# Optimization experiments

Measured on AMD Instinct MI355X. Metric: run time of the kernel, lower is better.

Reference implementation:

```python
import math
import jax, jax.numpy as jnp
import numpy as np

# ---- model dims ----
D = 4096          # hidden_size
N = 32            # num_attention_heads (== num_key_value_heads)
Q_LORA = 1536
KV_LORA = 512
QK_NOPE = 128
QK_ROPE = 64
QK_HEAD = QK_NOPE + QK_ROPE   # 192
V_HEAD = 128
EPS = 1e-6
T = 2048

# ---- yarn rope constants ----
ROPE_THETA = 10000.0
FACTOR = 40.0
ORIG_MAX = 4096
BETA_FAST = 32.0
BETA_SLOW = 1.0
MSCALE = 1.0
MSCALE_ALL_DIM = 1.0


def _yarn_get_mscale(scale, mscale):
    if scale <= 1.0:
        return 1.0
    return 0.1 * mscale * math.log(scale) + 1.0

# softmax scale: qk_head_dim^-0.5 * yarn_mscale^2 (rope_mscale_all_dim = 1.0)
YARN_MSCALE = _yarn_get_mscale(FACTOR, MSCALE_ALL_DIM)
SM_SCALE = QK_HEAD ** (-0.5) * YARN_MSCALE ** 2


def _yarn_cos_sin(positions):
    """DeepSeek yarn scaled rotary embeddings. positions: int [T]."""
    half = QK_ROPE // 2
    pow_ = np.arange(0, QK_ROPE, 2, dtype=np.float64) / QK_ROPE
    pos_freqs = ROPE_THETA ** pow_
    inv_extra = 1.0 / pos_freqs
    inv_inter = 1.0 / (FACTOR * pos_freqs)

    def corr_dim(n_rot):
        return (QK_ROPE * math.log(ORIG_MAX / (n_rot * 2 * math.pi))) / (2 * math.log(ROPE_THETA))

    low = max(math.floor(corr_dim(BETA_FAST)), 0)
    high = min(math.ceil(corr_dim(BETA_SLOW)), QK_ROPE - 1)
    ramp = np.clip((np.arange(half, dtype=np.float64) - low) / max(high - low, 1e-3), 0.0, 1.0)
    mask = 1.0 - ramp  # 1 where extrapolation
    inv_freq = inv_inter * (1.0 - mask) + inv_extra * mask
    inv_freq = jnp.asarray(inv_freq, jnp.float32)

    mscale_coef = _yarn_get_mscale(FACTOR, MSCALE) / _yarn_get_mscale(FACTOR, MSCALE_ALL_DIM)
    t = positions.astype(jnp.float32)
    freqs = t[:, None] * inv_freq[None, :]          # [T, half]
    return jnp.cos(freqs) * mscale_coef, jnp.sin(freqs) * mscale_coef


def _apply_rope(x_tnh, cos, sin):
    """Neox-style (split halves) rope. x: [T, N, QK_ROPE]; cos/sin: [T, half]."""
    half = QK_ROPE // 2
    x1, x2 = x_tnh[..., :half], x_tnh[..., half:]
    c, s = cos[:, None, :], sin[:, None, :]
    return jnp.concatenate([x1 * c - x2 * s, x1 * s + x2 * c], axis=-1)


def _rms_norm(x, scale, eps=EPS):
    var = jnp.mean(jnp.square(x), axis=-1, keepdims=True)
    return x * jax.lax.rsqrt(var + eps) * scale


def setup_inputs() -> dict:
    key = jax.random.key(0)
    ks = jax.random.split(key, 8)
    std = 0.02
    return {
        "x": jax.random.normal(ks[0], (T, D), jnp.float32),
        "positions": jnp.arange(T, dtype=jnp.int32),
        "w_q_down": jax.random.normal(ks[1], (D, Q_LORA), jnp.float32) * std,
        "q_norm_scale": jnp.ones((Q_LORA,), jnp.float32),
        "w_q_up": jax.random.normal(ks[2], (Q_LORA, N, QK_HEAD), jnp.float32) * std,
        "w_kv_down": jax.random.normal(ks[3], (D, KV_LORA + QK_ROPE), jnp.float32) * std,
        "kv_norm_scale": jnp.ones((KV_LORA,), jnp.float32),
        "w_kv_up": jax.random.normal(ks[4], (KV_LORA, N, QK_NOPE + V_HEAD), jnp.float32) * std,
        "w_o": jax.random.normal(ks[5], (N, V_HEAD, D), jnp.float32) * std,
    }


def reference(x, positions, w_q_down, q_norm_scale, w_q_up, w_kv_down,
              kv_norm_scale, w_kv_up, w_o):
    cos, sin = _yarn_cos_sin(positions)

    # ---- q projection (low rank) ----
    q_ta = _rms_norm(jnp.einsum('td,da->ta', x, w_q_down), q_norm_scale)
    q_tnh = jnp.einsum('ta,anh->tnh', q_ta, w_q_up)            # [T,N,192]
    q_rope = _apply_rope(q_tnh[..., QK_NOPE:], cos, sin)
    q_tnh = jnp.concatenate([q_tnh[..., :QK_NOPE], q_rope], axis=-1)

    # ---- kv projection (compressed latent) ----
    kv_sa = jnp.einsum('sd,da->sa', x, w_kv_down)              # [T, KV_LORA+64]
    k_rope = _apply_rope(kv_sa[:, None, KV_LORA:], cos, sin)   # [T,1,64]
    k_rope = jnp.broadcast_to(k_rope, (x.shape[0], N, QK_ROPE))
    kv_lat = _rms_norm(kv_sa[..., :KV_LORA], kv_norm_scale)
    kv_nope = jnp.einsum('sa,anh->snh', kv_lat, w_kv_up)       # [T,N,256]
    k_snh = jnp.concatenate([kv_nope[..., :QK_NOPE], k_rope], axis=-1)
    v_snh = kv_nope[..., QK_NOPE:]

    # ---- causal attention (prefill; padding to 128-multiple is a no-op) ----
    scores = jnp.einsum('tnh,snh->nts', q_tnh, k_snh) * SM_SCALE
    tpos = jnp.arange(x.shape[0])
    causal = tpos[:, None] >= tpos[None, :]
    scores = jnp.where(causal[None, :, :], scores, jnp.finfo(scores.dtype).min)
    probs = jax.nn.softmax(scores, axis=-1)
    out_tnh = jnp.einsum('nts,snh->tnh', probs, v_snh)

    # ---- output projection ----
    return jnp.einsum('tnh,nhd->td', out_tnh, w_o)
```

## Files before the change

kernel.cpp:

```cpp
#include <hip/hip_runtime.h>
#include <math.h>
#include <stdint.h>

#define T_    2048
#define D_    4096
#define NH_   32
#define QL_   1536
#define KVL_  512
#define ROPE_ 64
#define NOPE_ 128
#define HQK_  192
#define HV_   128
#define KVD_  576
#define NCAT_ 2112

typedef __bf16 bf16x8 __attribute__((ext_vector_type(8)));
typedef __bf16 bf16x4 __attribute__((ext_vector_type(4)));
typedef float f32x4 __attribute__((ext_vector_type(4)));

__device__ __forceinline__ void gload_lds16(const __bf16* g, __bf16* l) {
  __builtin_amdgcn_global_load_lds(
      (const __attribute__((address_space(1))) void*)g,
      (__attribute__((address_space(3))) void*)l, 16, 0, 0);
}

template <typename OutT>
__global__ __launch_bounds__(256, 3) void mfma_gemm_kernel(
    const __bf16* __restrict__ A, const __bf16* __restrict__ Bt,
    OutT* __restrict__ C, int M, int Ncols, int K) {
  __shared__ __bf16 As[128 * 64];
  __shared__ __bf16 Bs[128 * 64];
  const int tid = threadIdx.x;
  const int lane = tid & 63;
  const int w = tid >> 6;
  const int wm = w >> 1, wn = w & 1;
  const int lg = lane >> 4, lj = lane & 15;
  const int bm = blockIdx.y * 128;
  const int bn = blockIdx.x * 128;

  const __bf16* ga[4]; const __bf16* gb[4];
  int ldsoff[4];
  #pragma unroll
  for (int i = 0; i < 4; ++i) {
    int task = i * 256 + tid;
    int r = task >> 3, cl = task & 7;
    int cg = cl ^ (r & 7);
    ga[i] = A  + (size_t)(bm + r) * K + cg * 8;
    gb[i] = Bt + (size_t)(bn + r) * K + cg * 8;
    ldsoff[i] = (i * 256 + w * 64) * 8;
  }

  f32x4 acc[4][4];
  #pragma unroll
  for (int mi = 0; mi < 4; ++mi)
    #pragma unroll
    for (int ni = 0; ni < 4; ++ni) acc[mi][ni] = (f32x4){0.f, 0.f, 0.f, 0.f};

  for (int k0 = 0; k0 < K; k0 += 64) {
    __syncthreads();
    #pragma unroll
    for (int i = 0; i < 4; ++i) gload_lds16(ga[i] + k0, &As[ldsoff[i]]);
    #pragma unroll
    for (int i = 0; i < 4; ++i) gload_lds16(gb[i] + k0, &Bs[ldsoff[i]]);
    __syncthreads();
    #pragma unroll
    for (int kh = 0; kh < 2; ++kh) {
      bf16x8 af[4], bfr[4];
      #pragma unroll
      for (int i = 0; i < 4; ++i) {
        int ra = wm * 64 + i * 16 + lj;
        af[i] = *(const bf16x8*)&As[ra * 64 + ((((kh << 2) + lg) ^ (ra & 7)) << 3)];
      }
      #pragma unroll
      for (int i = 0; i < 4; ++i) {
        int rb = wn * 64 + i * 16 + lj;
        bfr[i] = *(const bf16x8*)&Bs[rb * 64 + ((((kh << 2) + lg) ^ (rb & 7)) << 3)];
      }
      #pragma unroll
      for (int mi = 0; mi < 4; ++mi)
        #pragma unroll
        for (int ni = 0; ni < 4; ++ni)
          acc[mi][ni] = __builtin_amdgcn_mfma_f32_16x16x32_bf16(af[mi], bfr[ni], acc[mi][ni], 0, 0, 0);
    }
  }

  #pragma unroll
  for (int mi = 0; mi < 4; ++mi) {
    #pragma unroll
    for (int r = 0; r < 4; ++r) {
      int row = bm + wm * 64 + mi * 16 + lg * 4 + r;
      #pragma unroll
      for (int ni = 0; ni < 4; ++ni) {
        int col = bn + wn * 64 + ni * 16 + lj;
        if (col < Ncols) C[(size_t)row * Ncols + col] = (OutT)acc[mi][ni][r];
      }
    }
  }
}

__global__ __launch_bounds__(256) void transpose_bf16_kernel(
    const float* __restrict__ B, __bf16* __restrict__ Bt, int K, int N) {
  __shared__ float tile[64][65];
  int n0 = blockIdx.x * 64, k0 = blockIdx.y * 64;
  int tid = threadIdx.x;
  int kr = tid >> 4, nc = (tid & 15) * 4;
  #pragma unroll
  for (int i = 0; i < 4; ++i) {
    int k = kr + i * 16;
    float4 v = make_float4(0.f, 0.f, 0.f, 0.f);
    if (n0 + nc < N) v = *(const float4*)(B + (size_t)(k0 + k) * N + n0 + nc);
    tile[k][nc + 0] = v.x; tile[k][nc + 1] = v.y;
    tile[k][nc + 2] = v.z; tile[k][nc + 3] = v.w;
  }
  __syncthreads();
  int nl = tid >> 4, k4 = (tid & 15) * 4;
  #pragma unroll
  for (int i = 0; i < 4; ++i) {
    int nn = nl + i * 16;
    bf16x4 o;
    o[0] = (__bf16)tile[k4 + 0][nn]; o[1] = (__bf16)tile[k4 + 1][nn];
    o[2] = (__bf16)tile[k4 + 2][nn]; o[3] = (__bf16)tile[k4 + 3][nn];
    *(bf16x4*)(Bt + (size_t)(n0 + nn) * K + k0 + k4) = o;
  }
}

__global__ __launch_bounds__(256) void conv_bf16_kernel(
    const float* __restrict__ in, __bf16* __restrict__ out, int n8) {
  int i = blockIdx.x * 256 + threadIdx.x;
  if (i >= n8) return;
  float4 a = *(const float4*)(in + (size_t)i * 8);
  float4 b = *(const float4*)(in + (size_t)i * 8 + 4);
  bf16x8 v;
  v[0] = (__bf16)a.x; v[1] = (__bf16)a.y; v[2] = (__bf16)a.z; v[3] = (__bf16)a.w;
  v[4] = (__bf16)b.x; v[5] = (__bf16)b.y; v[6] = (__bf16)b.z; v[7] = (__bf16)b.w;
  *(bf16x8*)(out + (size_t)i * 8) = v;
}

__global__ __launch_bounds__(256) void rmsnorm_bf16_kernel(
    const float* __restrict__ in, __bf16* __restrict__ out,
    const float* __restrict__ scale, int len, int in_stride) {
  int row = blockIdx.x;
  const float* x = in + (size_t)row * in_stride;
  __bf16* y = out + (size_t)row * len;
  float ss = 0.f;
  for (int i = threadIdx.x; i < len; i += 256) { float v = x[i]; ss += v * v; }
  __shared__ float red[4];
  #pragma unroll
  for (int o = 32; o > 0; o >>= 1) ss += __shfl_down(ss, o, 64);
  int wid = threadIdx.x >> 6, lane = threadIdx.x & 63;
  if (lane == 0) red[wid] = ss;
  __syncthreads();
  if (threadIdx.x == 0) {
    float t = red[0] + red[1] + red[2] + red[3];
    red[0] = 1.0f / sqrtf(t / (float)len + 1e-6f);
  }
  __syncthreads();
  float r = red[0];
  for (int i = threadIdx.x; i < len; i += 256) y[i] = (__bf16)(x[i] * r * scale[i]);
}

struct InvFreq { float f[32]; };
__global__ __launch_bounds__(256) void rope_table_kernel(
    const int* __restrict__ pos, float* __restrict__ cosT, float* __restrict__ sinT,
    InvFreq invf) {
  int idx = blockIdx.x * 256 + threadIdx.x;
  if (idx >= T_ * 32) return;
  int t = idx >> 5, i = idx & 31;
  float fr = (float)pos[t] * invf.f[i];
  cosT[idx] = cosf(fr);
  sinT[idx] = sinf(fr);
}

__global__ __launch_bounds__(256) void rope_q_kernel(
    __bf16* __restrict__ q, const float* __restrict__ cosT, const float* __restrict__ sinT) {
  int idx = blockIdx.x * 256 + threadIdx.x;
  if (idx >= T_ * NH_ * 32) return;
  int i = idx & 31;
  int tn = idx >> 5;
  int t = tn >> 5;
  __bf16* b = q + (size_t)tn * HQK_ + NOPE_;
  float x1 = (float)b[i], x2 = (float)b[i + 32];
  float c = cosT[t * 32 + i], s = sinT[t * 32 + i];
  b[i]      = (__bf16)(x1 * c - x2 * s);
  b[i + 32] = (__bf16)(x1 * s + x2 * c);
}

__global__ __launch_bounds__(256) void rope_k_kernel(
    const float* __restrict__ src, int stride, const float* __restrict__ cosT,
    const float* __restrict__ sinT, __bf16* __restrict__ k_rope) {
  int idx = blockIdx.x * 256 + threadIdx.x;
  if (idx >= T_ * 32) return;
  int t = idx >> 5, i = idx & 31;
  const float* b = src + (size_t)t * stride;
  float x1 = b[i], x2 = b[i + 32];
  float c = cosT[idx], s = sinT[idx];
  k_rope[t * 64 + i]      = (__bf16)(x1 * c - x2 * s);
  k_rope[t * 64 + i + 32] = (__bf16)(x1 * s + x2 * c);
}

__global__ __launch_bounds__(256) void prep_vt_kernel(
    const __bf16* __restrict__ kv_nopeb, __bf16* __restrict__ Vt) {
  __shared__ __bf16 tile[64][136];
  int s0 = blockIdx.x * 64;
  int n = blockIdx.y;
  int tid = threadIdx.x;
  #pragma unroll
  for (int i = 0; i < 4; ++i) {
    int idx = tid + i * 256;
    int s = idx >> 4, c = idx & 15;
    bf16x8 v = *(const bf16x8*)(kv_nopeb + ((size_t)(s0 + s) * NH_ + n) * 256 + NOPE_ + c * 8);
    *(bf16x8*)&tile[s][c * 8] = v;
  }
  __syncthreads();
  #pragma unroll
  for (int i = 0; i < 8; ++i) {
    int idx = tid + i * 256;
    int h = idx >> 4, s4 = (idx & 15) * 4;
    bf16x4 v;
    v[0] = tile[s4 + 0][h]; v[1] = tile[s4 + 1][h];
    v[2] = tile[s4 + 2][h]; v[3] = tile[s4 + 3][h];
    *(bf16x4*)(Vt + ((size_t)n * HV_ + h) * T_ + s0 + s4) = v;
  }
}

__global__ __launch_bounds__(256) void attn_mfma_kernel(
    const __bf16* __restrict__ q_tnh, const __bf16* __restrict__ kv_nopeb,
    const __bf16* __restrict__ k_rope, const __bf16* __restrict__ Vt,
    __bf16* __restrict__ attn_out, float sm_scale) {
  __shared__ __bf16 KsL[2][24 * 32 * 8];
  __shared__ __bf16 VsL[2][4 * 128 * 8];
  __shared__ __bf16 Ps[4][16 * 64];
  const int tid = threadIdx.x;
  const int lane = tid & 63;
  const int w = tid >> 6;
  const int id = blockIdx.x;
  const int j = id >> 3;
  const int qt = 31 - (j >> 2);
  const int n = (id & 7) * 4 + (j & 3);
  const int t0 = qt * 64;
  const int lg = lane >> 4;
  const int lj = lane & 15;
  const int rowbase = t0 + w * 16;

  const __bf16* kbase[3]; size_t kstep[3]; int klds[3];
  #pragma unroll
  for (int i = 0; i < 3; ++i) {
    int task = i * 256 + tid;
    int c = task >> 5, s = task & 31;
    if (c < 16) { kbase[i] = kv_nopeb + ((size_t)s * NH_ + n) * 256 + c * 8; kstep[i] = (size_t)32 * NH_ * 256; }
    else        { kbase[i] = k_rope + (size_t)s * ROPE_ + (c - 16) * 8;      kstep[i] = (size_t)32 * ROPE_; }
    klds[i] = (i * 256 + w * 64) * 8;
  }
  const __bf16* vbase[2]; int vlds[2];
  #pragma unroll
  for (int i = 0; i < 2; ++i) {
    int task = i * 256 + tid;
    int c = task >> 7, h = task & 127;
    vbase[i] = Vt + ((size_t)n * HV_ + h) * T_ + c * 8;
    vlds[i] = (i * 256 + w * 64) * 8;
  }

  #define STAGE(tileIdx, bufIdx)                                               \
    do {                                                                       \
      __bf16* kb_ = &KsL[bufIdx][0];                                           \
      __bf16* vb_ = &VsL[bufIdx][0];                                           \
      _Pragma("unroll")                                                        \
      for (int i_ = 0; i_ < 3; ++i_)                                           \
        gload_lds16(kbase[i_] + (size_t)(tileIdx) * kstep[i_], kb_ + klds[i_]);\
      _Pragma("unroll")                                                        \
      for (int i_ = 0; i_ < 2; ++i_)                                           \
        gload_lds16(vbase[i_] + (size_t)(tileIdx) * 32, vb_ + vlds[i_]);       \
    } while (0)

  STAGE(0, 0);

  bf16x8 qf[6];
  {
    int t = t0 + w * 16 + lj;
    const __bf16* qp = q_tnh + ((size_t)t * NH_ + n) * HQK_;
    #pragma unroll
    for (int kk = 0; kk < 6; ++kk) {
      bf16x8 raw = *(const bf16x8*)(qp + kk * 32 + lg * 8);
      bf16x8 v;
      #pragma unroll
      for (int i = 0; i < 8; ++i) v[i] = (__bf16)((float)raw[i] * sm_scale);
      qf[kk] = v;
    }
  }

  f32x4 O[8];
  #pragma unroll
  for (int nb = 0; nb < 8; ++nb) O[nb] = (f32x4){0.f, 0.f, 0.f, 0.f};
  float m_r[4], l_r[4];
  #pragma unroll
  for (int r = 0; r < 4; ++r) { m_r[r] = -1e30f; l_r[r] = 0.f; }

  __syncthreads();

  const int nst = 2 * (qt + 1);
  #pragma unroll 1
  for (int st = 0; st < nst; ++st) {
    const int s0 = st * 32;
    const int cur = st & 1;
    if (st + 1 < nst) STAGE(st + 1, cur ^ 1);
    const __bf16* kb = &KsL[cur][0];
    const __bf16* vb = &VsL[cur][0];

    if (s0 <= rowbase + 15) {
      f32x4 S[2];
      __builtin_amdgcn_s_setprio(1);
      #pragma unroll
      for (int sb = 0; sb < 2; ++sb) {
        f32x4 acc = (f32x4){0.f, 0.f, 0.f, 0.f};
        int srow = sb * 16 + lj;
        #pragma unroll
        for (int kk = 0; kk < 6; ++kk) {
          int c = kk * 4 + lg;
          bf16x8 b = *(const bf16x8*)&kb[(c * 32 + srow) * 8];
          acc = __builtin_amdgcn_mfma_f32_16x16x32_bf16(qf[kk], b, acc, 0, 0, 0);
        }
        S[sb] = acc;
      }
      __builtin_amdgcn_s_setprio(0);
      if (s0 + 31 > rowbase) {
        #pragma unroll
        for (int sb = 0; sb < 2; ++sb)
          #pragma unroll
          for (int r = 0; r < 4; ++r) {
            int row = rowbase + lg * 4 + r;
            int col = s0 + sb * 16 + lj;
            if (col > row) S[sb][r] = -1e30f;
          }
      }
      #pragma unroll
      for (int r = 0; r < 4; ++r) {
        float mx = fmaxf(S[0][r], S[1][r]);
        mx = fmaxf(mx, __shfl_xor(mx, 1));
        mx = fmaxf(mx, __shfl_xor(mx, 2));
        mx = fmaxf(mx, __shfl_xor(mx, 4));
        mx = fmaxf(mx, __shfl_xor(mx, 8));
        float mnew = fmaxf(m_r[r], mx);
        float corr = __expf(m_r[r] - mnew);
        m_r[r] = mnew;
        float psum = 0.f;
        #pragma unroll
        for (int sb = 0; sb < 2; ++sb) {
          float pp = __expf(S[sb][r] - mnew);
          S[sb][r] = pp;
          psum += pp;
        }
        l_r[r] = l_r[r] * corr + psum;
        #pragma unroll
        for (int nb = 0; nb < 8; ++nb) O[nb][r] = O[nb][r] * corr;
      }
      #pragma unroll
      for (int sb = 0; sb < 2; ++sb) {
        int sl = sb * 16 + lj;
        int c = sl >> 3;
        #pragma unroll
        for (int r = 0; r < 4; ++r) {
          int rw = lg * 4 + r;
          Ps[w][rw * 64 + ((c ^ (rw & 7)) << 3) + (sl & 7)] = (__bf16)S[sb][r];
        }
      }
      {
        bf16x8 pa = *(const bf16x8*)&Ps[w][lj * 64 + ((lg ^ (lj & 7)) << 3)];
        __builtin_amdgcn_s_setprio(1);
        #pragma unroll
        for (int nb = 0; nb < 8; ++nb) {
          int h = nb * 16 + lj;
          bf16x8 bv = *(const bf16x8*)&vb[(lg * 128 + h) * 8];
          O[nb] = __builtin_amdgcn_mfma_f32_16x16x32_bf16(pa, bv, O[nb], 0, 0, 0);
        }
        __builtin_amdgcn_s_setprio(0);
      }
    }
    __syncthreads();
  }

  #pragma unroll
  for (int r = 0; r < 4; ++r) {
    float lsum = l_r[r];
    lsum += __shfl_xor(lsum, 1);
    lsum += __shfl_xor(lsum, 2);
    lsum += __shfl_xor(lsum, 4);
    lsum += __shfl_xor(lsum, 8);
    float inv = 1.0f / lsum;
    int t = t0 + w * 16 + lg * 4 + r;
    __bf16* dst = attn_out + ((size_t)t * NH_ + n) * HV_;
    #pragma unroll
    for (int nb = 0; nb < 8; ++nb) dst[nb * 16 + lj] = (__bf16)(O[nb][r] * inv);
  }
  #undef STAGE
}

static void compute_inv_freq(float* out) {
  const double theta = 10000.0, factor = 40.0;
  const double PI = 3.14159265358979323846;
  const int rot = ROPE_;
  double low_d  = rot * log(4096.0 / (32.0 * 2.0 * PI)) / (2.0 * log(theta));
  double high_d = rot * log(4096.0 / ( 1.0 * 2.0 * PI)) / (2.0 * log(theta));
  double low = floor(low_d);  if (low < 0) low = 0;
  double high = ceil(high_d); if (high > rot - 1) high = rot - 1;
  for (int i = 0; i < 32; ++i) {
    double pf = pow(theta, (2.0 * i) / (double)rot);
    double inv_extra = 1.0 / pf;
    double inv_inter = 1.0 / (factor * pf);
    double ramp = ((double)i - low) / fmax(high - low, 0.001);
    ramp = fmin(fmax(ramp, 0.0), 1.0);
    double mask = 1.0 - ramp;
    out[i] = (float)(inv_inter * (1.0 - mask) + inv_extra * mask);
  }
}

extern "C" void kernel_launch(void* const* d_in, const int* in_sizes, int n_in,
                              void* d_out, int out_size, void* d_ws, size_t ws_size,
                              hipStream_t stream) {
  const float* x            = (const float*)d_in[0];
  const int*   positions    = (const int*)d_in[1];
  const float* w_q_down     = (const float*)d_in[2];
  const float* q_norm_scale = (const float*)d_in[3];
  const float* w_q_up       = (const float*)d_in[4];
  const float* w_kv_down    = (const float*)d_in[5];
  const float* kv_norm_scale= (const float*)d_in[6];
  const float* w_kv_up      = (const float*)d_in[7];
  const float* w_o          = (const float*)d_in[8];
  float* out = (float*)d_out;

  float* ws = (float*)d_ws;
  float*  cosT     = ws;
  float*  sinT     = ws + 65536;
  float*  cat      = ws + 131072;
  __bf16* xb       = (__bf16*)(ws + 4456448);
  __bf16* Bt_cat   = (__bf16*)(ws + 8650752);
  __bf16* Bt_qu    = (__bf16*)(ws + 13107200);
  __bf16* Bt_kvu   = (__bf16*)(ws + 17825792);
  __bf16* q_tab    = (__bf16*)(ws + 19922944);
  __bf16* kv_latb  = (__bf16*)(ws + 21495808);
  __bf16* k_ropeb  = (__bf16*)(ws + 22020096);
  __bf16* q_tnhb   = (__bf16*)(ws + 22085632);
  __bf16* kv_nopeb = (__bf16*)(ws + 28377088);
  __bf16* Vt       = (__bf16*)(ws + 13107200);
  __bf16* attn_ob  = (__bf16*)(ws + 17825792);
  __bf16* Bt_o     = (__bf16*)(ws + 4456448);
  (void)ws_size; (void)n_in; (void)in_sizes; (void)out_size;

  InvFreq invf;
  compute_inv_freq(invf.f);
  double ym = 0.1 * log(40.0) + 1.0;
  float sm_scale = (float)(ym * ym / sqrt((double)HQK_));

  rope_table_kernel<<<(T_ * 32 + 255) / 256, 256, 0, stream>>>(positions, cosT, sinT, invf);
  conv_bf16_kernel<<<T_ * D_ / 8 / 256, 256, 0, stream>>>(x, xb, T_ * D_ / 8);
  transpose_bf16_kernel<<<dim3(QL_ / 64, D_ / 64), 256, 0, stream>>>(w_q_down, Bt_cat, D_, QL_);
  transpose_bf16_kernel<<<dim3(KVD_ / 64, D_ / 64), 256, 0, stream>>>(w_kv_down, Bt_cat + (size_t)QL_ * D_, D_, KVD_);
  transpose_bf16_kernel<<<dim3(NH_ * HQK_ / 64, QL_ / 64), 256, 0, stream>>>(w_q_up, Bt_qu, QL_, NH_ * HQK_);
  transpose_bf16_kernel<<<dim3(NH_ * 256 / 64, KVL_ / 64), 256, 0, stream>>>(w_kv_up, Bt_kvu, KVL_, NH_ * 256);

  mfma_gemm_kernel<float><<<dim3((NCAT_ + 127) / 128, T_ / 128), 256, 0, stream>>>(xb, Bt_cat, cat, T_, NCAT_, D_);

  rmsnorm_bf16_kernel<<<T_, 256, 0, stream>>>(cat, q_tab, q_norm_scale, QL_, NCAT_);
  mfma_gemm_kernel<__bf16><<<dim3(NH_ * HQK_ / 128, T_ / 128), 256, 0, stream>>>(q_tab, Bt_qu, q_tnhb, T_, NH_ * HQK_, QL_);
  rope_q_kernel<<<(T_ * NH_ * 32 + 255) / 256, 256, 0, stream>>>(q_tnhb, cosT, sinT);

  rmsnorm_bf16_kernel<<<T_, 256, 0, stream>>>(cat + QL_, kv_latb, kv_norm_scale, KVL_, NCAT_);
  rope_k_kernel<<<(T_ * 32 + 255) / 256, 256, 0, stream>>>(cat + QL_ + KVL_, NCAT_, cosT, sinT, k_ropeb);
  mfma_gemm_kernel<__bf16><<<dim3(NH_ * 256 / 128, T_ / 128), 256, 0, stream>>>(kv_latb, Bt_kvu, kv_nopeb, T_, NH_ * 256, KVL_);

  prep_vt_kernel<<<dim3(T_ / 64, NH_), 256, 0, stream>>>(kv_nopeb, Vt);
  attn_mfma_kernel<<<1024, 256, 0, stream>>>(q_tnhb, kv_nopeb, k_ropeb, Vt, attn_ob, sm_scale);

  transpose_bf16_kernel<<<dim3(D_ / 64, NH_ * HV_ / 64), 256, 0, stream>>>(w_o, Bt_o, NH_ * HV_, D_);
  mfma_gemm_kernel<float><<<dim3(D_ / 128, T_ / 128), 256, 0, stream>>>(attn_ob, Bt_o, out, T_, D_, NH_ * HV_);
}
```

Baseline: 428.1 us.

## Widen attention KV tile to 64, skip unchanged rescales, and swizzle GEMM blocks

The attention kernel now processes 64 keys per iteration instead of 32. K stays double-buffered, and V is loaded into a single buffer within the same iteration, with an extra barrier before the PV MFMAs. The online-softmax correction of O and l is skipped when no row max increases anywhere in the wave. Separately, the GEMM kernel remaps block IDs in groups of 8 to improve L2 locality. In exchange, V load latency is no longer hidden by prefetch, the diagonal tile handles a full 64-wide mask, and the extra barrier adds synchronization.

```diff
diff --git a/kernel.cpp b/kernel.cpp
--- a/kernel.cpp
+++ b/kernel.cpp
@@ -35,8 +35,13 @@
   const int w = tid >> 6;
   const int wm = w >> 1, wn = w & 1;
   const int lg = lane >> 4, lj = lane & 15;
-  const int bm = blockIdx.y * 128;
-  const int bn = blockIdx.x * 128;
+
+  const int gx = gridDim.x;
+  const int nwg = gx * gridDim.y;
+  int id = blockIdx.y * gx + blockIdx.x;
+  if ((nwg & 7) == 0) id = (id & 7) * (nwg >> 3) + (id >> 3);
+  const int bm = (id / gx) * 128;
+  const int bn = (id % gx) * 128;
 
   const __bf16* ga[4]; const __bf16* gb[4];
   int ldsoff[4];
@@ -227,8 +232,8 @@
     const __bf16* __restrict__ q_tnh, const __bf16* __restrict__ kv_nopeb,
     const __bf16* __restrict__ k_rope, const __bf16* __restrict__ Vt,
     __bf16* __restrict__ attn_out, float sm_scale) {
-  __shared__ __bf16 KsL[2][24 * 32 * 8];
-  __shared__ __bf16 VsL[2][4 * 128 * 8];
+  __shared__ __bf16 KsL[2][24 * 64 * 8];
+  __shared__ __bf16 Vs[8 * 128 * 8];
   __shared__ __bf16 Ps[4][16 * 64];
   const int tid = threadIdx.x;
   const int lane = tid & 63;
@@ -242,37 +247,39 @@
   const int lj = lane & 15;
   const int rowbase = t0 + w * 16;
 
-  const __bf16* kbase[3]; size_t kstep[3]; int klds[3];
-  #pragma unroll
-  for (int i = 0; i < 3; ++i) {
+  const __bf16* kbase[6]; size_t kstep[6]; int klds[6];
+  #pragma unroll
+  for (int i = 0; i < 6; ++i) {
     int task = i * 256 + tid;
-    int c = task >> 5, s = task & 31;
-    if (c < 16) { kbase[i] = kv_nopeb + ((size_t)s * NH_ + n) * 256 + c * 8; kstep[i] = (size_t)32 * NH_ * 256; }
-    else        { kbase[i] = k_rope + (size_t)s * ROPE_ + (c - 16) * 8;      kstep[i] = (size_t)32 * ROPE_; }
+    int c = task >> 6, s = task & 63;
+    if (c < 16) { kbase[i] = kv_nopeb + ((size_t)s * NH_ + n) * 256 + c * 8; kstep[i] = (size_t)64 * NH_ * 256; }
+    else        { kbase[i] = k_rope + (size_t)s * ROPE_ + (c - 16) * 8;      kstep[i] = (size_t)64 * ROPE_; }
     klds[i] = (i * 256 + w * 64) * 8;
   }
-  const __bf16* vbase[2]; int vlds[2];
-  #pragma unroll
-  for (int i = 0; i < 2; ++i) {
+  const __bf16* vbase[4]; int vlds[4];
+  #pragma unroll
+  for (int i = 0; i < 4; ++i) {
     int task = i * 256 + tid;
     int c = task >> 7, h = task & 127;
     vbase[i] = Vt + ((size_t)n * HV_ + h) * T_ + c * 8;
     vlds[i] = (i * 256 + w * 64) * 8;
   }
 
-  #define STAGE(tileIdx, bufIdx)                                               \
+  #define STAGE_K(tileIdx, bufIdx)                                             \
     do {                                                                       \
       __bf16* kb_ = &KsL[bufIdx][0];                                           \
-      __bf16* vb_ = &VsL[bufIdx][0];                                           \
       _Pragma("unroll")                                                        \
-      for (int i_ = 0; i_ < 3; ++i_)                                           \
+      for (int i_ = 0; i_ < 6; ++i_)                                           \
         gload_lds16(kbase[i_] + (size_t)(tileIdx) * kstep[i_], kb_ + klds[i_]);\
+    } while (0)
+  #define STAGE_V(tileIdx)                                                     \
+    do {                                                                       \
       _Pragma("unroll")                                                        \
-      for (int i_ = 0; i_ < 2; ++i_)                                           \
-        gload_lds16(vbase[i_] + (size_t)(tileIdx) * 32, vb_ + vlds[i_]);       \
+      for (int i_ = 0; i_ < 4; ++i_)                                           \
+        gload_lds16(vbase[i_] + (size_t)(tileIdx) * 64, &Vs[0] + vlds[i_]);    \
     } while (0)
 
-  STAGE(0, 0);
+  STAGE_K(0, 0);
 
   bf16x8 qf[6];
   {
@@ -297,84 +304,97 @@
 
   __syncthreads();
 
-  const int nst = 2 * (qt + 1);
+  const int nst = qt + 1;
   #pragma unroll 1
   for (int st = 0; st < nst; ++st) {
-    const int s0 = st * 32;
+    const int s0 = st * 64;
     const int cur = st & 1;
-    if (st + 1 < nst) STAGE(st + 1, cur ^ 1);
+    if (st + 1 < nst) STAGE_K(st + 1, cur ^ 1);
+    STAGE_V(st);
     const __bf16* kb = &KsL[cur][0];
-    const __bf16* vb = &VsL[cur][0];
-
-    if (s0 <= rowbase + 15) {
-      f32x4 S[2];
-      __builtin_amdgcn_s_setprio(1);
-      #pragma unroll
-      for (int sb = 0; sb < 2; ++sb) {
-        f32x4 acc = (f32x4){0.f, 0.f, 0.f, 0.f};
-        int srow = sb * 16 + lj;
+
+    f32x4 S[4];
+    __builtin_amdgcn_s_setprio(1);
+    #pragma unroll
+    for (int sb = 0; sb < 4; ++sb) {
+      f32x4 acc = (f32x4){0.f, 0.f, 0.f, 0.f};
+      int srow = sb * 16 + lj;
+      #pragma unroll
+      for (int kk = 0; kk < 6; ++kk) {
+        int c = kk * 4 + lg;
+        bf16x8 b = *(const bf16x8*)&kb[(c * 64 + srow) * 8];
+        acc = __builtin_amdgcn_mfma_f32_16x16x32_bf16(qf[kk], b, acc, 0, 0, 0);
+      }
+      S[sb] = acc;
+    }
+    __builtin_amdgcn_s_setprio(0);
+    if (st == qt) {
+      #pragma unroll
+      for (int sb = 0; sb < 4; ++sb)
         #pragma unroll
-        for (int kk = 0; kk < 6; ++kk) {
-          int c = kk * 4 + lg;
-          bf16x8 b = *(const bf16x8*)&kb[(c * 32 + srow) * 8];
-          acc = __builtin_amdgcn_mfma_f32_16x16x32_bf16(qf[kk], b, acc, 0, 0, 0);
+        for (int r = 0; r < 4; ++r) {
+          int row = rowbase + lg * 4 + r;
+          int col = s0 + sb * 16 + lj;
+          if (col > row) S[sb][r] = -1e30f;
         }
-        S[sb] = acc;
-      }
-      __builtin_amdgcn_s_setprio(0);
-      if (s0 + 31 > rowbase) {
-        #pragma unroll
-        for (int sb = 0; sb < 2; ++sb)
-          #pragma unroll
-          for (int r = 0; r < 4; ++r) {
-            int row = rowbase + lg * 4 + r;
-            int col = s0 + sb * 16 + lj;
-            if (col > row) S[sb][r] = -1e30f;
-          }
-      }
+    }
+    float mx[4];
+    #pragma unroll
+    for (int r = 0; r < 4; ++r) {
+      float m2 = fmaxf(fmaxf(S[0][r], S[1][r]), fmaxf(S[2][r], S[3][r]));
+      m2 = fmaxf(m2, __shfl_xor(m2, 1));
+      m2 = fmaxf(m2, __shfl_xor(m2, 2));
+      m2 = fmaxf(m2, __shfl_xor(m2, 4));
+      m2 = fmaxf(m2, __shfl_xor(m2, 8));
+      mx[r] = m2;
+    }
+    int need = (mx[0] > m_r[0]) | (mx[1] > m_r[1]) | (mx[2] > m_r[2]) | (mx[3] > m_r[3]);
+    if (__any(need)) {
       #pragma unroll
       for (int r = 0; r < 4; ++r) {
-        float mx = fmaxf(S[0][r], S[1][r]);
-        mx = fmaxf(mx, __shfl_xor(mx, 1));
-        mx = fmaxf(mx, __shfl_xor(mx, 2));
-        mx = fmaxf(mx, __shfl_xor(mx, 4));
-        mx = fmaxf(mx, __shfl_xor(mx, 8));
-        float mnew = fmaxf(m_r[r], mx);
+        float mnew = fmaxf(m_r[r], mx[r]);
         float corr = __expf(m_r[r] - mnew);
         m_r[r] = mnew;
-        float psum = 0.f;
-        #pragma unroll
-        for (int sb = 0; sb < 2; ++sb) {
-          float pp = __expf(S[sb][r] - mnew);
-          S[sb][r] = pp;
-          psum += pp;
-        }
-        l_r[r] = l_r[r] * corr + psum;
+        l_r[r] *= corr;
         #pragma unroll
         for (int nb = 0; nb < 8; ++nb) O[nb][r] = O[nb][r] * corr;
       }
-      #pragma unroll
-      for (int sb = 0; sb < 2; ++sb) {
-        int sl = sb * 16 + lj;
-        int c = sl >> 3;
-        #pragma unroll
-        for (int r = 0; r < 4; ++r) {
-          int rw = lg * 4 + r;
-          Ps[w][rw * 64 + ((c ^ (rw & 7)) << 3) + (sl & 7)] = (__bf16)S[sb][r];
-        }
-      }
-      {
-        bf16x8 pa = *(const bf16x8*)&Ps[w][lj * 64 + ((lg ^ (lj & 7)) << 3)];
-        __builtin_amdgcn_s_setprio(1);
-        #pragma unroll
-        for (int nb = 0; nb < 8; ++nb) {
-          int h = nb * 16 + lj;
-          bf16x8 bv = *(const bf16x8*)&vb[(lg * 128 + h) * 8];
-          O[nb] = __builtin_amdgcn_mfma_f32_16x16x32_bf16(pa, bv, O[nb], 0, 0, 0);
-        }
-        __builtin_amdgcn_s_setprio(0);
-      }
-    }
+    }
+    #pragma unroll
+    for (int r = 0; r < 4; ++r) {
+      float psum = 0.f;
+      #pragma unroll
+      for (int sb = 0; sb < 4; ++sb) {
+        float pp = __expf(S[sb][r] - m_r[r]);
+        S[sb][r] = pp;
+        psum += pp;
+      }
+      l_r[r] += psum;
+    }
+    #pragma unroll
+    for (int sb = 0; sb < 4; ++sb) {
+      int sl = sb * 16 + lj;
+      int c = sl >> 3;
+      #pragma unroll
+      for (int r = 0; r < 4; ++r) {
+        int rw = lg * 4 + r;
+        Ps[w][rw * 64 + ((c ^ (rw & 7)) << 3) + (sl & 7)] = (__bf16)S[sb][r];
+      }
+    }
+    __syncthreads();
+    __builtin_amdgcn_s_setprio(1);
+    #pragma unroll
+    for (int kk = 0; kk < 2; ++kk) {
+      int ca = kk * 4 + lg;
+      bf16x8 pa = *(const bf16x8*)&Ps[w][lj * 64 + ((ca ^ (lj & 7)) << 3)];
+      #pragma unroll
+      for (int nb = 0; nb < 8; ++nb) {
+        int h = nb * 16 + lj;
+        bf16x8 bv = *(const bf16x8*)&Vs[(ca * 128 + h) * 8];
+        O[nb] = __builtin_amdgcn_mfma_f32_16x16x32_bf16(pa, bv, O[nb], 0, 0, 0);
+      }
+    }
+    __builtin_amdgcn_s_setprio(0);
     __syncthreads();
   }
 
@@ -391,7 +411,8 @@
     #pragma unroll
     for (int nb = 0; nb < 8; ++nb) dst[nb * 16 + lj] = (__bf16)(O[nb][r] * inv);
   }
-  #undef STAGE
+  #undef STAGE_K
+  #undef STAGE_V
 }
 
 static void compute_inv_freq(float* out) {
```

New measurement: 422.4 us. No clear change (-1.3%).
